# Performance work log

Measured on AMD Instinct MI355X. Metric: run time of the kernel, lower is better.

The kernel has to match this reference:

```python
import jax, jax.numpy as jnp
import numpy as np

B, N, C = 8, 1024, 768
H = 12
HD = C // H
RANK = 8
SCALE = HD ** -0.5


def setup_inputs() -> dict:
    key = jax.random.key(0)
    ks = jax.random.split(key, 12)
    s = C ** -0.5
    inp = {
        'x': jax.random.normal(ks[0], (B, N, C), jnp.float32),
        'w_qkv': jax.random.normal(ks[1], (3 * C, C), jnp.float32) * s,
        'b_qkv': jax.random.normal(ks[2], (3 * C,), jnp.float32) * 0.02,
        'w_proj': jax.random.normal(ks[3], (C, C), jnp.float32) * s,
        'b_proj': jax.random.normal(ks[4], (C,), jnp.float32) * 0.02,
        # LoRA A matrices (kaiming-uniform-ish); B matrices are zero at init,
        # but use small nonzero values so the adapter path is exercised.
        'q_a': jax.random.normal(ks[5], (RANK, C), jnp.float32) * s,
        'q_b': jax.random.normal(ks[6], (C, RANK), jnp.float32) * 0.01,
        'k_a': jax.random.normal(ks[7], (RANK, C), jnp.float32) * s,
        'k_b': jax.random.normal(ks[8], (C, RANK), jnp.float32) * 0.01,
        'v_a': jax.random.normal(ks[9], (RANK, C), jnp.float32) * s,
        'v_b': jax.random.normal(ks[10], (C, RANK), jnp.float32) * 0.01,
        'o_a': jax.random.normal(ks[11], (RANK, C), jnp.float32) * s,
        'o_b': jax.random.normal(jax.random.fold_in(key, 99), (C, RANK), jnp.float32) * 0.01,
    }
    return inp


def _lora(x, wa, wb):
    # x:[B,N,C], wa:[r,C], wb:[C,r] -> [B,N,C]
    return jnp.einsum('bnr,cr->bnc', jnp.einsum('bnc,rc->bnr', x, wa), wb)


def reference(x, w_qkv, b_qkv, w_proj, b_proj, q_a, q_b, k_a, k_b, v_a, v_b, o_a, o_b):
    # QKV projection + fused LoRA slice-adds
    qkv = jnp.einsum('bnc,dc->bnd', x, w_qkv) + b_qkv  # [B,N,3C]
    q = qkv[:, :, :C] + _lora(x, q_a, q_b)
    k = qkv[:, :, C:2 * C] + _lora(x, k_a, k_b)
    v = qkv[:, :, 2 * C:] + _lora(x, v_a, v_b)
    # [B,H,N,HD]
    q = q.reshape(B, N, H, HD).transpose(0, 2, 1, 3)
    k = k.reshape(B, N, H, HD).transpose(0, 2, 1, 3)
    v = v.reshape(B, N, H, HD).transpose(0, 2, 1, 3)
    attn = jnp.einsum('bhqd,bhkd->bhqk', q, k) * SCALE
    attn = jax.nn.softmax(attn, axis=-1)  # dropout is identity in eval
    o = jnp.einsum('bhqk,bhkd->bhqd', attn, v)
    o = o.transpose(0, 2, 1, 3).reshape(B, N, C)
    out = jnp.einsum('bnc,dc->bnd', o, w_proj) + b_proj + _lora(o, o_a, o_b)
    return out
```

## Files before the change

kernel.cpp:

```cpp
#include <hip/hip_runtime.h>

typedef __attribute__((ext_vector_type(8))) short short8;
typedef __attribute__((ext_vector_type(4))) float f32x4;
typedef __attribute__((ext_vector_type(4))) unsigned short u16x4;
typedef __attribute__((ext_vector_type(4))) unsigned int u32x4;

#define MFMA16(a,b,c) __builtin_amdgcn_mfma_f32_16x16x32_bf16((a),(b),(c),0,0,0)

#define QSCALE 0.1803368801f

__device__ __forceinline__ unsigned short f2bf(float f) {
  unsigned int x = __float_as_uint(f);
  x += 0x7fffu + ((x >> 16) & 1u);
  return (unsigned short)(x >> 16);
}
__device__ __forceinline__ void gload16(const unsigned short* g, unsigned short* l) {
  __builtin_amdgcn_global_load_lds(
      (const __attribute__((address_space(1))) unsigned int*)g,
      (__attribute__((address_space(3))) unsigned int*)l, 16, 0, 0);
}
__device__ __forceinline__ unsigned int cvtpk(float a, float b) {
  unsigned int r;
  asm("v_cvt_pk_bf16_f32 %0, %1, %2" : "=v"(r) : "v"(a), "v"(b));
  return r;
}


__global__ __launch_bounds__(256) void prep(
    const float* __restrict__ x,
    const float* __restrict__ w_qkv,
    const float* __restrict__ w_proj,
    const float* __restrict__ q_a, const float* __restrict__ q_b,
    const float* __restrict__ k_a, const float* __restrict__ k_b,
    const float* __restrict__ v_a, const float* __restrict__ v_b,
    const float* __restrict__ o_a, const float* __restrict__ o_b,
    unsigned short* __restrict__ xf,
    unsigned short* __restrict__ wqkv_eff,
    unsigned short* __restrict__ wproj_eff)
{
  int bid = blockIdx.x;
  if (bid < 6144) {
    int i4 = (bid * 256 + threadIdx.x) * 4;
    int m  = i4 / 768;
    int k4 = i4 - m * 768;
    f32x4 v = *(const f32x4*)&x[i4];
    u16x4 o;
    o.x = f2bf(v.x); o.y = f2bf(v.y); o.z = f2bf(v.z); o.w = f2bf(v.w);
    int kb = k4 >> 5, qd = (k4 >> 3) & 3, j0 = k4 & 7;
    size_t idx = ((size_t)(kb * 512 + (m >> 4)) << 9) +
                 (((qd << 4) + (m & 15)) << 3) + j0;
    *(u16x4*)&xf[idx] = o;
    return;
  }
  const int QKV = 2304 * 768;
  int idx = (bid - 6144) * 256 + threadIdx.x;
  if (idx < QKV) {
    int n = idx / 768, c = idx - n * 768;
    int sec = n / 768;
    int nr = n - sec * 768;
    const float* a; const float* b;
    if (sec == 0)      { a = q_a; b = q_b; }
    else if (sec == 1) { a = k_a; b = k_b; }
    else               { a = v_a; b = v_b; }
    float acc = w_qkv[idx];
    #pragma unroll
    for (int r = 0; r < 8; r++)
      acc += b[nr * 8 + r] * a[r * 768 + c];
    wqkv_eff[idx] = f2bf(acc);
  } else {
    int i2 = idx - QKV;
    int n = i2 / 768, c = i2 - n * 768;
    float acc = w_proj[i2];
    #pragma unroll
    for (int r = 0; r < 8; r++)
      acc += o_b[n * 8 + r] * o_a[r * 768 + c];
    wproj_eff[i2] = f2bf(acc);
  }
}

__global__ __launch_bounds__(256) void gemm_bt(
    const unsigned short* __restrict__ Af,
    const unsigned short* __restrict__ W,
    const float* __restrict__ bias,
    unsigned short* __restrict__ out0,
    unsigned short* __restrict__ out1,
    unsigned short* __restrict__ out2,
    float* __restrict__ outf,
    int K, int Ncols, int mode)
{
  __shared__ alignas(16) unsigned short Ws[64][72];
  const int tid  = threadIdx.x;
  const int wave = tid >> 6;
  const int lane = tid & 63;
  const int quad = lane >> 4;
  const int l16  = lane & 15;
  const int m0 = blockIdx.x * 128;
  const int n0 = blockIdx.y * 64;
  const int M16b = (m0 >> 4) + wave * 2;

  int wr[2], wc[2];
  #pragma unroll
  for (int i = 0; i < 2; i++) { int f = tid + i * 256; wr[i] = f >> 3; wc[i] = (f & 7) << 3; }

  f32x4 wreg[2];
  #pragma unroll
  for (int i = 0; i < 2; i++)
    wreg[i] = *(const f32x4*)&W[(size_t)(n0 + wr[i]) * K + wc[i]];

  short8 aCur[2][2], aNxt[2][2] = {};
  #pragma unroll
  for (int t = 0; t < 2; t++)
    #pragma unroll
    for (int ks = 0; ks < 2; ks++)
      aCur[t][ks] = *(const short8*)&Af[((size_t)(ks * 512 + M16b + t) << 9) + (lane << 3)];

  f32x4 acc[2][4] = {};

  for (int k0 = 0; k0 < K; k0 += 64) {
    __syncthreads();
    #pragma unroll
    for (int i = 0; i < 2; i++) *(f32x4*)&Ws[wr[i]][wc[i]] = wreg[i];
    __syncthreads();
    if (k0 + 64 < K) {
      #pragma unroll
      for (int i = 0; i < 2; i++)
        wreg[i] = *(const f32x4*)&W[(size_t)(n0 + wr[i]) * K + k0 + 64 + wc[i]];
      const int kbn = (k0 + 64) >> 5;
      #pragma unroll
      for (int t = 0; t < 2; t++)
        #pragma unroll
        for (int ks = 0; ks < 2; ks++)
          aNxt[t][ks] = *(const short8*)&Af[((size_t)((kbn + ks) * 512 + M16b + t) << 9) + (lane << 3)];
    }
    #pragma unroll
    for (int ks = 0; ks < 2; ks++) {
      const int kk = ks * 32 + quad * 8;
      short8 b0 = *(const short8*)&Ws[l16][kk];
      short8 b1 = *(const short8*)&Ws[16 + l16][kk];
      short8 b2 = *(const short8*)&Ws[32 + l16][kk];
      short8 b3 = *(const short8*)&Ws[48 + l16][kk];
      acc[0][0] = MFMA16(aCur[0][ks], b0, acc[0][0]);
      acc[0][1] = MFMA16(aCur[0][ks], b1, acc[0][1]);
      acc[0][2] = MFMA16(aCur[0][ks], b2, acc[0][2]);
      acc[0][3] = MFMA16(aCur[0][ks], b3, acc[0][3]);
      acc[1][0] = MFMA16(aCur[1][ks], b0, acc[1][0]);
      acc[1][1] = MFMA16(aCur[1][ks], b1, acc[1][1]);
      acc[1][2] = MFMA16(aCur[1][ks], b2, acc[1][2]);
      acc[1][3] = MFMA16(aCur[1][ks], b3, acc[1][3]);
    }
    #pragma unroll
    for (int t = 0; t < 2; t++)
      #pragma unroll
      for (int ks = 0; ks < 2; ks++)
        aCur[t][ks] = aNxt[t][ks];
  }

  float bv[4];
  #pragma unroll
  for (int j = 0; j < 4; j++) bv[j] = bias[n0 + j * 16 + l16];

  if (mode == 0) {
    const int sec = n0 / 768;
    const int h   = (n0 % 768) >> 6;
    unsigned short* dst = (sec == 0) ? out0 : ((sec == 1) ? out1 : out2);
    const float scl = (sec == 0) ? QSCALE : 1.0f;
    #pragma unroll
    for (int rg = 0; rg < 2; rg++) {
      #pragma unroll
      for (int r = 0; r < 4; r++) {
        int m  = m0 + wave * 32 + rg * 16 + quad * 4 + r;
        int b  = m >> 10, np = m & 1023;
        int bh = b * 12 + h;
        int s = (np & 35) | ((np & 12) << 1) | ((np & 16) >> 2);
        #pragma unroll
        for (int j = 0; j < 4; j++) {
          int d = j * 16 + l16;
          float v = (acc[rg][j][r] + bv[j]) * scl;
          if (sec == 0) {
            dst[((size_t)bh << 16) + ((size_t)np << 6) + d] = f2bf(v);
          } else if (sec == 1) {
            size_t kidx = ((size_t)((np >> 4) * 2 + (d >> 5)) << 9) +
                          ((((d >> 3) & 3) * 16 + (np & 15)) << 3) + (d & 7);
            dst[((size_t)bh << 16) + kidx] = f2bf(v);
          } else {
            size_t vidx = ((size_t)(((np >> 6) * 2 + (s >> 5)) * 4 + (d >> 4)) << 9) +
                          ((((s >> 3) & 3) * 16 + (d & 15)) << 3) + (s & 7);
            dst[((size_t)bh << 16) + vidx] = f2bf(v);
          }
        }
      }
    }
  } else {
    #pragma unroll
    for (int rg = 0; rg < 2; rg++) {
      #pragma unroll
      for (int r = 0; r < 4; r++) {
        int m = m0 + wave * 32 + rg * 16 + quad * 4 + r;
        #pragma unroll
        for (int j = 0; j < 4; j++)
          outf[(size_t)m * Ncols + n0 + j * 16 + l16] = acc[rg][j][r] + bv[j];
      }
    }
  }
}

__global__ __launch_bounds__(256) void attn(
    const unsigned short* __restrict__ q,
    const unsigned short* __restrict__ k,
    const unsigned short* __restrict__ vt,
    unsigned short* __restrict__ of)
{
  __shared__ alignas(16) unsigned short Ks2[2][4096];
  __shared__ alignas(16) unsigned short Vs2[2][4096];
  const int tid  = threadIdx.x;
  const int wave = tid >> 6;
  const int lane = tid & 63;
  const int quad = lane >> 4;
  const int l16  = lane & 15;
  const int bh = blockIdx.x;
  const int q0 = blockIdx.y * 64;
  const unsigned short* qb = q  + ((size_t)bh << 16);
  const unsigned short* kb = k  + ((size_t)bh << 16);
  const unsigned short* vb = vt + ((size_t)bh << 16);

  const int t8 = tid * 8;
  gload16(kb + t8,        &Ks2[0][t8]);
  gload16(kb + 2048 + t8, &Ks2[0][2048 + t8]);
  gload16(vb + t8,        &Vs2[0][t8]);
  gload16(vb + 2048 + t8, &Vs2[0][2048 + t8]);

  short8 bq[2];
  #pragma unroll
  for (int ks = 0; ks < 2; ks++)
    bq[ks] = *(const short8*)&qb[((size_t)(q0 + wave * 16 + l16) << 6) +
                                 ks * 32 + quad * 8];

  union { u32x4 w; short8 h; } onesu;
  onesu.w.x = 0x3F803F80u; onesu.w.y = 0x3F803F80u;
  onesu.w.z = 0x3F803F80u; onesu.w.w = 0x3F803F80u;
  const short8 onesb = onesu.h;

  f32x4 Oacc[4] = {};
  f32x4 lacc = {};

  union PAW { u32x4 w; short8 h; };

  for (int kt = 0; kt < 16; kt++) {
    const int p = kt & 1;
    __syncthreads();
    if (kt < 15) {
      const unsigned short* gkn = kb + (kt + 1) * 4096 + t8;
      const unsigned short* gvn = vb + (kt + 1) * 4096 + t8;
      gload16(gkn,        &Ks2[1 - p][t8]);
      gload16(gkn + 2048, &Ks2[1 - p][2048 + t8]);
      gload16(gvn,        &Vs2[1 - p][t8]);
      gload16(gvn + 2048, &Vs2[1 - p][2048 + t8]);
    }

    f32x4 s[4] = {};
    #pragma unroll
    for (int ks = 0; ks < 2; ks++) {
      const unsigned short* lk = &Ks2[p][ks * 512 + lane * 8];
      short8 a0 = *(const short8*)&lk[0];
      short8 a1 = *(const short8*)&lk[1024];
      short8 a2 = *(const short8*)&lk[2048];
      short8 a3 = *(const short8*)&lk[3072];
      s[0] = MFMA16(a0, bq[ks], s[0]);
      s[1] = MFMA16(a1, bq[ks], s[1]);
      s[2] = MFMA16(a2, bq[ks], s[2]);
      s[3] = MFMA16(a3, bq[ks], s[3]);
    }

    f32x4 e[4];
    #pragma unroll
    for (int i = 0; i < 4; i++) {
      e[i].x = exp2f(s[i].x);
      e[i].y = exp2f(s[i].y);
      e[i].z = exp2f(s[i].z);
      e[i].w = exp2f(s[i].w);
    }
    short8 pa[2];
    #pragma unroll
    for (int ks = 0; ks < 2; ks++) {
      PAW pw;
      pw.w.x = cvtpk(e[2 * ks].x,     e[2 * ks].y);
      pw.w.y = cvtpk(e[2 * ks].z,     e[2 * ks].w);
      pw.w.z = cvtpk(e[2 * ks + 1].x, e[2 * ks + 1].y);
      pw.w.w = cvtpk(e[2 * ks + 1].z, e[2 * ks + 1].w);
      pa[ks] = pw.h;
    }

    #pragma unroll
    for (int ks = 0; ks < 2; ks++) {
      const unsigned short* lv = &Vs2[p][ks * 2048 + lane * 8];
      short8 v0 = *(const short8*)&lv[0];
      short8 v1 = *(const short8*)&lv[512];
      short8 v2 = *(const short8*)&lv[1024];
      short8 v3 = *(const short8*)&lv[1536];
      Oacc[0] = MFMA16(pa[ks], v0, Oacc[0]);
      Oacc[1] = MFMA16(pa[ks], v1, Oacc[1]);
      Oacc[2] = MFMA16(pa[ks], v2, Oacc[2]);
      Oacc[3] = MFMA16(pa[ks], v3, Oacc[3]);
      lacc    = MFMA16(pa[ks], onesb, lacc);
    }
  }

  const int b = bh / 12, h = bh - (bh / 12) * 12;
  #pragma unroll
  for (int r = 0; r < 4; r++) {
    float inv = 1.0f / lacc[r];
    int np  = q0 + wave * 16 + quad * 4 + r;
    int M16 = b * 64 + (np >> 4);
    int l16m = np & 15;
    #pragma unroll
    for (int j = 0; j < 4; j++) {
      int col = h * 64 + j * 16 + l16;
      int kb2 = col >> 5;
      int qc  = (col >> 3) & 3;
      size_t idx = ((size_t)(kb2 * 512 + M16) << 9) +
                   ((qc * 16 + l16m) << 3) + (l16 & 7);
      of[idx] = f2bf(Oacc[j][r] * inv);
    }
  }
}

extern "C" void kernel_launch(void* const* d_in, const int* in_sizes, int n_in,
                              void* d_out, int out_size, void* d_ws, size_t ws_size,
                              hipStream_t stream) {
  const float* x      = (const float*)d_in[0];
  const float* w_qkv  = (const float*)d_in[1];
  const float* b_qkv  = (const float*)d_in[2];
  const float* w_proj = (const float*)d_in[3];
  const float* b_proj = (const float*)d_in[4];
  const float* q_a    = (const float*)d_in[5];
  const float* q_b    = (const float*)d_in[6];
  const float* k_a    = (const float*)d_in[7];
  const float* k_b    = (const float*)d_in[8];
  const float* v_a    = (const float*)d_in[9];
  const float* v_b    = (const float*)d_in[10];
  const float* o_a    = (const float*)d_in[11];
  const float* o_b    = (const float*)d_in[12];

  char* ws = (char*)d_ws;
  unsigned short* wqkv_eff  = (unsigned short*)(ws + 0);
  unsigned short* wproj_eff = (unsigned short*)(ws + 3538944);
  unsigned short* xf        = (unsigned short*)(ws + 4718592);
  unsigned short* qd        = (unsigned short*)(ws + 17301504);
  unsigned short* kd        = (unsigned short*)(ws + 29884416);
  unsigned short* vtd       = (unsigned short*)(ws + 42467328);
  unsigned short* of        = xf;

  prep<<<dim3(6144 + 9216), dim3(256), 0, stream>>>(
      x, w_qkv, w_proj, q_a, q_b, k_a, k_b, v_a, v_b, o_a, o_b,
      xf, wqkv_eff, wproj_eff);

  gemm_bt<<<dim3(64, 36), dim3(256), 0, stream>>>(
      xf, wqkv_eff, b_qkv, qd, kd, vtd, nullptr, 768, 2304, 0);

  attn<<<dim3(96, 16), dim3(256), 0, stream>>>(qd, kd, vtd, of);

  gemm_bt<<<dim3(64, 12), dim3(256), 0, stream>>>(
      of, wproj_eff, b_proj, nullptr, nullptr, nullptr, (float*)d_out, 768, 768, 1);
}
```

Baseline: 215.8 us.

## Pre-tile GEMM weights into MFMA fragment layout and double-buffer via direct-to-LDS loads

The weight-merge kernel now writes the LoRA-merged bf16 weights in a tiled layout: 16-row by 32-column blocks of 512 elements, arranged to match the MFMA B-operand fragment. The GEMM loads these tiles straight into a double-buffered LDS array with global_load_lds, so it no longer stages them in registers and writes them to padded shared memory. Each k-step now needs one barrier instead of two, and the next tile's load overlaps the current tile's MFMAs. The cost is scattered writes in the merge kernel and a reliance on the async LDS loads being complete by the time the barrier is crossed.

```diff
diff --git a/kernel.cpp b/kernel.cpp
--- a/kernel.cpp
+++ b/kernel.cpp
@@ -66,7 +66,9 @@
     #pragma unroll
     for (int r = 0; r < 8; r++)
       acc += b[nr * 8 + r] * a[r * 768 + c];
-    wqkv_eff[idx] = f2bf(acc);
+    size_t widx = ((size_t)((n >> 4) * 24 + (c >> 5)) << 9) +
+                  ((((c >> 3) & 3) * 16 + (n & 15)) << 3) + (c & 7);
+    wqkv_eff[widx] = f2bf(acc);
   } else {
     int i2 = idx - QKV;
     int n = i2 / 768, c = i2 - n * 768;
@@ -74,13 +76,15 @@
     #pragma unroll
     for (int r = 0; r < 8; r++)
       acc += o_b[n * 8 + r] * o_a[r * 768 + c];
-    wproj_eff[i2] = f2bf(acc);
+    size_t widx = ((size_t)((n >> 4) * 24 + (c >> 5)) << 9) +
+                  ((((c >> 3) & 3) * 16 + (n & 15)) << 3) + (c & 7);
+    wproj_eff[widx] = f2bf(acc);
   }
 }
 
 __global__ __launch_bounds__(256) void gemm_bt(
     const unsigned short* __restrict__ Af,
-    const unsigned short* __restrict__ W,
+    const unsigned short* __restrict__ Wf,
     const float* __restrict__ bias,
     unsigned short* __restrict__ out0,
     unsigned short* __restrict__ out1,
@@ -88,7 +92,7 @@
     float* __restrict__ outf,
     int K, int Ncols, int mode)
 {
-  __shared__ alignas(16) unsigned short Ws[64][72];
+  __shared__ alignas(16) unsigned short Wl[2][4096];
   const int tid  = threadIdx.x;
   const int wave = tid >> 6;
   const int lane = tid & 63;
@@ -97,15 +101,15 @@
   const int m0 = blockIdx.x * 128;
   const int n0 = blockIdx.y * 64;
   const int M16b = (m0 >> 4) + wave * 2;
-
-  int wr[2], wc[2];
-  #pragma unroll
-  for (int i = 0; i < 2; i++) { int f = tid + i * 256; wr[i] = f >> 3; wc[i] = (f & 7) << 3; }
-
-  f32x4 wreg[2];
-  #pragma unroll
-  for (int i = 0; i < 2; i++)
-    wreg[i] = *(const f32x4*)&W[(size_t)(n0 + wr[i]) * K + wc[i]];
+  const int nt0 = n0 >> 4;
+  const int NKB = K >> 5;
+
+  #pragma unroll
+  for (int a = 0; a < 2; a++) {
+    const int i = a * 4 + wave;
+    gload16(Wf + ((size_t)((nt0 + (i >> 1)) * NKB + (i & 1)) << 9) + (lane << 3),
+            &Wl[0][(i << 9) + (lane << 3)]);
+  }
 
   short8 aCur[2][2], aNxt[2][2] = {};
   #pragma unroll
@@ -115,17 +119,19 @@
       aCur[t][ks] = *(const short8*)&Af[((size_t)(ks * 512 + M16b + t) << 9) + (lane << 3)];
 
   f32x4 acc[2][4] = {};
-
-  for (int k0 = 0; k0 < K; k0 += 64) {
+  const int nkc = K >> 6;
+
+  for (int kc = 0; kc < nkc; kc++) {
+    const int p = kc & 1;
     __syncthreads();
-    #pragma unroll
-    for (int i = 0; i < 2; i++) *(f32x4*)&Ws[wr[i]][wc[i]] = wreg[i];
-    __syncthreads();
-    if (k0 + 64 < K) {
-      #pragma unroll
-      for (int i = 0; i < 2; i++)
-        wreg[i] = *(const f32x4*)&W[(size_t)(n0 + wr[i]) * K + k0 + 64 + wc[i]];
-      const int kbn = (k0 + 64) >> 5;
+    if (kc + 1 < nkc) {
+      #pragma unroll
+      for (int a = 0; a < 2; a++) {
+        const int i = a * 4 + wave;
+        gload16(Wf + ((size_t)((nt0 + (i >> 1)) * NKB + (kc + 1) * 2 + (i & 1)) << 9) + (lane << 3),
+                &Wl[1 - p][(i << 9) + (lane << 3)]);
+      }
+      const int kbn = (kc + 1) * 2;
       #pragma unroll
       for (int t = 0; t < 2; t++)
         #pragma unroll
@@ -134,11 +140,10 @@
     }
     #pragma unroll
     for (int ks = 0; ks < 2; ks++) {
-      const int kk = ks * 32 + quad * 8;
-      short8 b0 = *(const short8*)&Ws[l16][kk];
-      short8 b1 = *(const short8*)&Ws[16 + l16][kk];
-      short8 b2 = *(const short8*)&Ws[32 + l16][kk];
-      short8 b3 = *(const short8*)&Ws[48 + l16][kk];
+      short8 b0 = *(const short8*)&Wl[p][((0 * 2 + ks) << 9) + (lane << 3)];
+      short8 b1 = *(const short8*)&Wl[p][((1 * 2 + ks) << 9) + (lane << 3)];
+      short8 b2 = *(const short8*)&Wl[p][((2 * 2 + ks) << 9) + (lane << 3)];
+      short8 b3 = *(const short8*)&Wl[p][((3 * 2 + ks) << 9) + (lane << 3)];
       acc[0][0] = MFMA16(aCur[0][ks], b0, acc[0][0]);
       acc[0][1] = MFMA16(aCur[0][ks], b1, acc[0][1]);
       acc[0][2] = MFMA16(aCur[0][ks], b2, acc[0][2]);
```

After: 218.6 us. No clear change (+1.3%).
